# Performance work log

Measured on AMD Instinct MI355X. Metric: run time of the kernel, lower is better.

## Reference

```python
import jax, jax.numpy as jnp
import numpy as np

B, S, H = 64, 512, 768
NUM_BD = 5
N_CLASSES = 9
N_REGIONS = 4096
GAMMA = 0.3


def setup_inputs() -> dict:
    key = jax.random.key(0)
    ks = jax.random.split(key, 11)
    return {
        "word_repr": jax.random.normal(ks[0], (B, S, H), dtype=jnp.float32),
        "W_s": jax.random.normal(ks[1], (H, NUM_BD), dtype=jnp.float32) * 0.02,
        "b_s": jax.random.normal(ks[2], (NUM_BD,), dtype=jnp.float32) * 0.02,
        "W_r": jax.random.normal(ks[3], (H, N_CLASSES), dtype=jnp.float32) * 0.02,
        "b_r": jax.random.normal(ks[4], (N_CLASSES,), dtype=jnp.float32) * 0.02,
        "bd_tgt": jax.random.randint(ks[5], (B, S), 0, NUM_BD),
        "seg": jax.random.randint(ks[6], (B, S), 0, 2),
        "region_starts": jax.random.randint(ks[7], (N_REGIONS,), 0, 495),
        "region_lengths": jax.random.randint(ks[8], (N_REGIONS,), 0, 16),
        "region_batch": jax.random.randint(ks[9], (N_REGIONS,), 0, B),
        "region_labels": jax.random.randint(ks[10], (N_REGIONS,), 0, N_CLASSES),
    }


def reference(word_repr, W_s, b_s, W_r, b_r, bd_tgt, seg,
              region_starts, region_lengths, region_batch, region_labels):
    dt = word_repr.dtype
    b, s, h = word_repr.shape

    # sentence boundary logits [B,S,5]
    sent_out = jnp.einsum('bsh,hk->bsk', word_repr, W_s) + b_s

    # --- region mean pooling via exclusive prefix sums (fused segment-mean) ---
    cs = jnp.concatenate(
        [jnp.zeros((b, 1, h), dt), jnp.cumsum(word_repr, axis=1)], axis=1)  # [B,S+1,H]
    ends = region_starts + region_lengths  # inclusive end index
    seg_sum = cs[region_batch, ends + 1] - cs[region_batch, region_starts]  # [R,H]
    lens = (region_lengths + 1).astype(dt)
    region_repr = seg_sum / lens[:, None]

    # region classification + cross-entropy (mean)
    region_logits = region_repr @ W_r + b_r  # [R,C]
    logp_r = jax.nn.log_softmax(region_logits, axis=-1)
    ent_loss = -jnp.mean(
        jnp.take_along_axis(logp_r, region_labels[:, None], axis=1)[:, 0])

    # boundary loss: masked mean NLL with one-hot targets
    logp_s = jax.nn.log_softmax(sent_out.reshape(-1, NUM_BD), axis=-1)
    nll = -jnp.take_along_axis(logp_s, bd_tgt.reshape(-1, 1), axis=1)[:, 0]
    mask = seg.reshape(-1).astype(dt)
    bd_loss = jnp.sum(mask * nll) / (jnp.sum(mask) + 1e-6)

    return GAMMA * ent_loss + (1.0 - GAMMA) * bd_loss
```

## Files before the change

kernel.cpp:

```cpp
#include <hip/hip_runtime.h>

#define BB 64
#define SS 512
#define HH 768
#define HH4 (HH / 4)
#define NBD 5
#define NC 9
#define NR 4096
#define NB_BD 2048
#define NB_RG 1024
#define NBLK (NB_BD + NB_RG)

__global__ __launch_bounds__(256) void fused_kernel(
    const float* __restrict__ wr, const float* __restrict__ Ws,
    const float* __restrict__ bs, const int* __restrict__ tgt,
    const int* __restrict__ seg,
    const float* __restrict__ Wr, const float* __restrict__ br,
    const int* __restrict__ rstart, const int* __restrict__ rlen,
    const int* __restrict__ rbatch, const int* __restrict__ rlabel,
    float2* __restrict__ bd_part, float* __restrict__ rnll)
{
    const int tid  = threadIdx.x;
    const int wid  = tid >> 6;
    const int lane = tid & 63;
    const int bid  = blockIdx.x;

    if (bid % 3 != 0) {
        const int bb = bid - bid / 3 - 1;
        const int gw = bb * 4 + wid;

        float wreg[3][4][NBD];
        #pragma unroll
        for (int j = 0; j < 3; ++j) {
            const float4* wp = (const float4*)(Ws + (4 * lane + 256 * j) * NBD);
            #pragma unroll
            for (int p = 0; p < 5; ++p) {
                const float4 f = wp[p];
                const float vv[4] = {f.x, f.y, f.z, f.w};
                #pragma unroll
                for (int q = 0; q < 4; ++q) {
                    const int flat = 4 * p + q;
                    wreg[j][flat / NBD][flat % NBD] = vv[q];
                }
            }
        }
        const float b0 = bs[0], b1 = bs[1], b2 = bs[2], b3 = bs[3], b4 = bs[4];

        float nll_sum = 0.f, msk_sum = 0.f;

        #pragma unroll
        for (int i = 0; i < 4; ++i) {
            const int token = gw + 8192 * i;
            const float4* row4 = (const float4*)(wr + (size_t)token * HH);

            float4 v[3];
            #pragma unroll
            for (int j = 0; j < 3; ++j) v[j] = row4[lane + 64 * j];

            float dot[NBD] = {0.f, 0.f, 0.f, 0.f, 0.f};
            #pragma unroll
            for (int j = 0; j < 3; ++j) {
                const float x[4] = {v[j].x, v[j].y, v[j].z, v[j].w};
                #pragma unroll
                for (int e = 0; e < 4; ++e)
                    #pragma unroll
                    for (int k = 0; k < NBD; ++k)
                        dot[k] += x[e] * wreg[j][e][k];
            }

            #pragma unroll
            for (int k = 0; k < NBD; ++k)
                #pragma unroll
                for (int off = 32; off; off >>= 1)
                    dot[k] += __shfl_xor(dot[k], off);

            if (lane == 0) {
                float l[NBD] = {dot[0] + b0, dot[1] + b1, dot[2] + b2,
                                dot[3] + b3, dot[4] + b4};
                float m = l[0];
                #pragma unroll
                for (int k = 1; k < NBD; ++k) m = fmaxf(m, l[k]);
                float ssum = 0.f;
                #pragma unroll
                for (int k = 0; k < NBD; ++k) ssum += expf(l[k] - m);
                const float lse = logf(ssum);
                const int   t   = tgt[token];
                const float msk = (float)seg[token];
                nll_sum += msk * (-(l[t] - m - lse));
                msk_sum += msk;
            }
        }

        __shared__ float s_n[4], s_m[4];
        if (lane == 0) { s_n[wid] = nll_sum; s_m[wid] = msk_sum; }
        __syncthreads();
        if (tid == 0) {
            bd_part[bb] = make_float2(s_n[0] + s_n[1] + s_n[2] + s_n[3],
                                      s_m[0] + s_m[1] + s_m[2] + s_m[3]);
        }
    } else {
        const int r = (bid / 3) * 4 + wid;

        const int   start = rstart[r];
        const int   len   = rlen[r] + 1;
        const int   b     = rbatch[r];
        const float inv   = 1.0f / (float)len;

        const float4* base =
            (const float4*)wr + ((size_t)b * SS + start) * HH4;

        float4 m0 = {0.f, 0.f, 0.f, 0.f};
        float4 m1 = {0.f, 0.f, 0.f, 0.f};
        float4 m2 = {0.f, 0.f, 0.f, 0.f};

        #pragma unroll 2
        for (int row = 0; row < len; ++row) {
            const float4* p = base + (size_t)row * HH4;
            const float4 u0 = p[lane];
            const float4 u1 = p[lane + 64];
            const float4 u2 = p[lane + 128];
            m0.x += u0.x; m0.y += u0.y; m0.z += u0.z; m0.w += u0.w;
            m1.x += u1.x; m1.y += u1.y; m1.z += u1.z; m1.w += u1.w;
            m2.x += u2.x; m2.y += u2.y; m2.z += u2.z; m2.w += u2.w;
        }

        float part[NC];
        #pragma unroll
        for (int c = 0; c < NC; ++c) part[c] = 0.f;

        const float mv[3][4] = {{m0.x * inv, m0.y * inv, m0.z * inv, m0.w * inv},
                                {m1.x * inv, m1.y * inv, m1.z * inv, m1.w * inv},
                                {m2.x * inv, m2.y * inv, m2.z * inv, m2.w * inv}};
        #pragma unroll
        for (int g = 0; g < 3; ++g) {
            const int f = lane + 64 * g;
            const float4* wv = (const float4*)(Wr + (size_t)4 * f * NC);
            #pragma unroll
            for (int j = 0; j < 9; ++j) {
                const float4 x = wv[j];
                const float vv[4] = {x.x, x.y, x.z, x.w};
                #pragma unroll
                for (int q = 0; q < 4; ++q) {
                    const int flat = 4 * j + q;
                    part[flat % NC] += mv[g][flat / NC] * vv[q];
                }
            }
        }

        #pragma unroll
        for (int c = 0; c < NC; ++c)
            #pragma unroll
            for (int off = 32; off; off >>= 1)
                part[c] += __shfl_xor(part[c], off);

        if (lane == 0) {
            float l[NC];
            #pragma unroll
            for (int c = 0; c < NC; ++c) l[c] = part[c] + br[c];
            float mx = l[0];
            #pragma unroll
            for (int c = 1; c < NC; ++c) mx = fmaxf(mx, l[c]);
            float ssum = 0.f;
            #pragma unroll
            for (int c = 0; c < NC; ++c) ssum += expf(l[c] - mx);
            const float lse = logf(ssum);
            const int   t   = rlabel[r];
            rnll[r] = -(l[t] - mx - lse);
        }
    }
}

__global__ __launch_bounds__(256) void fin_kernel(
    const float2* __restrict__ bdp, const float* __restrict__ rnll,
    float* __restrict__ out)
{
    const int tid  = threadIdx.x;
    const int wid  = tid >> 6;
    const int lane = tid & 63;

    double a = 0.0, c = 0.0, e = 0.0;
    for (int i = tid; i < NB_BD; i += 256) {
        const float2 p = bdp[i];
        a += (double)p.x;
        c += (double)p.y;
    }
    for (int i = tid; i < NR; i += 256) e += (double)rnll[i];

    #pragma unroll
    for (int off = 32; off; off >>= 1) {
        a += __shfl_xor(a, off);
        c += __shfl_xor(c, off);
        e += __shfl_xor(e, off);
    }

    __shared__ double sa[4], sc[4], se[4];
    if (lane == 0) { sa[wid] = a; sc[wid] = c; se[wid] = e; }
    __syncthreads();

    if (tid == 0) {
        const double A = sa[0] + sa[1] + sa[2] + sa[3];
        const double C = sc[0] + sc[1] + sc[2] + sc[3];
        const double E = se[0] + se[1] + se[2] + se[3];
        const float ent = (float)(E / (double)NR);
        const float bd  = (float)(A / (C + 1e-6));
        out[0] = 0.3f * ent + 0.7f * bd;
    }
}

extern "C" void kernel_launch(void* const* d_in, const int* in_sizes, int n_in,
                              void* d_out, int out_size, void* d_ws, size_t ws_size,
                              hipStream_t stream)
{
    const float* wr     = (const float*)d_in[0];
    const float* Ws     = (const float*)d_in[1];
    const float* bs     = (const float*)d_in[2];
    const float* Wr     = (const float*)d_in[3];
    const float* br     = (const float*)d_in[4];
    const int*   tgt    = (const int*)d_in[5];
    const int*   seg    = (const int*)d_in[6];
    const int*   rstart = (const int*)d_in[7];
    const int*   rlen   = (const int*)d_in[8];
    const int*   rbatch = (const int*)d_in[9];
    const int*   rlabel = (const int*)d_in[10];

    float2* bdp  = (float2*)d_ws;
    float*  rnll = (float*)((char*)d_ws + NB_BD * sizeof(float2));

    fused_kernel<<<NBLK, 256, 0, stream>>>(wr, Ws, bs, tgt, seg,
                                           Wr, br, rstart, rlen, rbatch, rlabel,
                                           bdp, rnll);
    fin_kernel<<<1, 256, 0, stream>>>(bdp, rnll, (float*)d_out);
}
```

Measured before the change: 190.9 us.

## Skip masked tokens and split boundary dot across four threads with LDS weights

```diff
diff --git a/kernel.cpp b/kernel.cpp
--- a/kernel.cpp
+++ b/kernel.cpp
@@ -1,15 +1,15 @@
 #include <hip/hip_runtime.h>
 
-#define BB 64
 #define SS 512
 #define HH 768
-#define HH4 (HH / 4)
+#define HH4 192
 #define NBD 5
 #define NC 9
 #define NR 4096
-#define NB_BD 2048
 #define NB_RG 1024
-#define NBLK (NB_BD + NB_RG)
+#define NB_BD 512
+#define NBLK (NB_RG + NB_BD)
+#define WS_LDS_SZ (HH * NBD + 24)
 
 __global__ __launch_bounds__(256) void fused_kernel(
     const float* __restrict__ wr, const float* __restrict__ Ws,
@@ -25,81 +25,11 @@
     const int lane = tid & 63;
     const int bid  = blockIdx.x;
 
-    if (bid % 3 != 0) {
-        const int bb = bid - bid / 3 - 1;
-        const int gw = bb * 4 + wid;
-
-        float wreg[3][4][NBD];
-        #pragma unroll
-        for (int j = 0; j < 3; ++j) {
-            const float4* wp = (const float4*)(Ws + (4 * lane + 256 * j) * NBD);
-            #pragma unroll
-            for (int p = 0; p < 5; ++p) {
-                const float4 f = wp[p];
-                const float vv[4] = {f.x, f.y, f.z, f.w};
-                #pragma unroll
-                for (int q = 0; q < 4; ++q) {
-                    const int flat = 4 * p + q;
-                    wreg[j][flat / NBD][flat % NBD] = vv[q];
-                }
-            }
-        }
-        const float b0 = bs[0], b1 = bs[1], b2 = bs[2], b3 = bs[3], b4 = bs[4];
-
-        float nll_sum = 0.f, msk_sum = 0.f;
-
-        #pragma unroll
-        for (int i = 0; i < 4; ++i) {
-            const int token = gw + 8192 * i;
-            const float4* row4 = (const float4*)(wr + (size_t)token * HH);
-
-            float4 v[3];
-            #pragma unroll
-            for (int j = 0; j < 3; ++j) v[j] = row4[lane + 64 * j];
-
-            float dot[NBD] = {0.f, 0.f, 0.f, 0.f, 0.f};
-            #pragma unroll
-            for (int j = 0; j < 3; ++j) {
-                const float x[4] = {v[j].x, v[j].y, v[j].z, v[j].w};
-                #pragma unroll
-                for (int e = 0; e < 4; ++e)
-                    #pragma unroll
-                    for (int k = 0; k < NBD; ++k)
-                        dot[k] += x[e] * wreg[j][e][k];
-            }
-
-            #pragma unroll
-            for (int k = 0; k < NBD; ++k)
-                #pragma unroll
-                for (int off = 32; off; off >>= 1)
-                    dot[k] += __shfl_xor(dot[k], off);
-
-            if (lane == 0) {
-                float l[NBD] = {dot[0] + b0, dot[1] + b1, dot[2] + b2,
-                                dot[3] + b3, dot[4] + b4};
-                float m = l[0];
-                #pragma unroll
-                for (int k = 1; k < NBD; ++k) m = fmaxf(m, l[k]);
-                float ssum = 0.f;
-                #pragma unroll
-                for (int k = 0; k < NBD; ++k) ssum += expf(l[k] - m);
-                const float lse = logf(ssum);
-                const int   t   = tgt[token];
-                const float msk = (float)seg[token];
-                nll_sum += msk * (-(l[t] - m - lse));
-                msk_sum += msk;
-            }
-        }
-
-        __shared__ float s_n[4], s_m[4];
-        if (lane == 0) { s_n[wid] = nll_sum; s_m[wid] = msk_sum; }
-        __syncthreads();
-        if (tid == 0) {
-            bd_part[bb] = make_float2(s_n[0] + s_n[1] + s_n[2] + s_n[3],
-                                      s_m[0] + s_m[1] + s_m[2] + s_m[3]);
-        }
-    } else {
-        const int r = (bid / 3) * 4 + wid;
+    __shared__ float ws_lds[WS_LDS_SZ];
+    __shared__ float s_n[4], s_m[4];
+
+    if (bid < NB_RG) {
+        const int r = bid * 4 + wid;
 
         const int   start = rstart[r];
         const int   len   = rlen[r] + 1;
@@ -113,7 +43,7 @@
         float4 m1 = {0.f, 0.f, 0.f, 0.f};
         float4 m2 = {0.f, 0.f, 0.f, 0.f};
 
-        #pragma unroll 2
+        #pragma unroll 4
         for (int row = 0; row < len; ++row) {
             const float4* p = base + (size_t)row * HH4;
             const float4 u0 = p[lane];
@@ -140,9 +70,9 @@
                 const float4 x = wv[j];
                 const float vv[4] = {x.x, x.y, x.z, x.w};
                 #pragma unroll
-                for (int q = 0; q < 4; ++q) {
-                    const int flat = 4 * j + q;
-                    part[flat % NC] += mv[g][flat / NC] * vv[q];
+                for (int qq = 0; qq < 4; ++qq) {
+                    const int flat = 4 * j + qq;
+                    part[flat % NC] += mv[g][flat / NC] * vv[qq];
                 }
             }
         }
@@ -166,6 +96,72 @@
             const float lse = logf(ssum);
             const int   t   = rlabel[r];
             rnll[r] = -(l[t] - mx - lse);
+        }
+    } else {
+        const int bb = bid - NB_RG;
+
+        for (int i = tid; i < HH * NBD; i += 256)
+            ws_lds[i + (i / 960) * 8] = Ws[i];
+        __syncthreads();
+
+        const int gl    = bb * 256 + tid;
+        const int token = gl >> 2;
+        const int q     = gl & 3;
+        const int seg_t = seg[token];
+
+        float dot[NBD] = {0.f, 0.f, 0.f, 0.f, 0.f};
+
+        if (seg_t != 0) {
+            const float4* row4 =
+                (const float4*)(wr + (size_t)token * HH) + q * 48;
+            const float* wsb = ws_lds + 968 * q;
+            #pragma unroll 4
+            for (int jj = 0; jj < 48; ++jj) {
+                const float4 v = row4[jj];
+                const float* wp = wsb + 20 * jj;
+                const float x[4] = {v.x, v.y, v.z, v.w};
+                #pragma unroll
+                for (int e = 0; e < 4; ++e)
+                    #pragma unroll
+                    for (int k = 0; k < NBD; ++k)
+                        dot[k] += x[e] * wp[e * NBD + k];
+            }
+        }
+
+        #pragma unroll
+        for (int k = 0; k < NBD; ++k) {
+            dot[k] += __shfl_xor(dot[k], 1);
+            dot[k] += __shfl_xor(dot[k], 2);
+        }
+
+        float nll = 0.f, msk = 0.f;
+        if (q == 0 && seg_t != 0) {
+            float l[NBD];
+            #pragma unroll
+            for (int k = 0; k < NBD; ++k) l[k] = dot[k] + bs[k];
+            float m = l[0];
+            #pragma unroll
+            for (int k = 1; k < NBD; ++k) m = fmaxf(m, l[k]);
+            float ssum = 0.f;
+            #pragma unroll
+            for (int k = 0; k < NBD; ++k) ssum += expf(l[k] - m);
+            const float lse = logf(ssum);
+            const int   t   = tgt[token];
+            nll = -(l[t] - m - lse);
+            msk = 1.0f;
+        }
+
+        #pragma unroll
+        for (int off = 32; off; off >>= 1) {
+            nll += __shfl_xor(nll, off);
+            msk += __shfl_xor(msk, off);
+        }
+
+        if (lane == 0) { s_n[wid] = nll; s_m[wid] = msk; }
+        __syncthreads();
+        if (tid == 0) {
+            bd_part[bb] = make_float2(s_n[0] + s_n[1] + s_n[2] + s_n[3],
+                                      s_m[0] + s_m[1] + s_m[2] + s_m[3]);
         }
     }
 }
```

Result: faster. 187.1 us (-2.0%).
